# Performance work log

Measured on AMD Instinct MI355X. Metric: run time of the kernel, lower is better.

Reference implementation:

```python
import jax, jax.numpy as jnp
import numpy as np

B, S, IN_DIM = 2048, 65, 256
H, L = 8, 256


def setup_inputs() -> dict:
    key = jax.random.key(0)
    ks = jax.random.split(key, 8)
    return {
        "x": jax.random.normal(ks[0], (B, S, IN_DIM), dtype=jnp.float32),
        "Wq": jax.random.normal(ks[1], (H, IN_DIM, L), dtype=jnp.float32),
        "Wk": jax.random.normal(ks[2], (H, IN_DIM, L), dtype=jnp.float32),
        "Wv": jax.random.normal(ks[3], (H, IN_DIM, L), dtype=jnp.float32),
        "W": jax.random.normal(ks[4], (H, L, 1), dtype=jnp.float32),
        "O": jax.random.normal(ks[5], (H * L, IN_DIM), dtype=jnp.float32),
        "P": jax.random.normal(ks[6], (S - 1, IN_DIM), dtype=jnp.float32),
        "bias": jax.random.normal(ks[7], (H,), dtype=jnp.float32),
    }


def reference(x, Wq, Wk, Wv, W, O, P, bias):
    origin = x[:, 0, :]                       # [B, D]
    walk = x[:, 1:, :]                        # [B, S-1, D]
    origin_seq = origin[:, None, :] + P       # [B, S-1, D]

    # per-head sigmoid projections, vectorized over heads
    k = jax.nn.sigmoid(jnp.einsum('bsd,hdl->bhsl', origin_seq, Wk))
    q = jax.nn.sigmoid(jnp.einsum('bsd,hdl->bhsl', walk, Wq))
    v = jax.nn.sigmoid(jnp.einsum('bsd,hdl->bhsl', walk, Wv))

    edge = jnp.cos(k * q) + bias[None, :, None, None]       # [B,H,S-1,L]
    score = jnp.einsum('bhsl,hl->bhs', edge, W[..., 0])      # [B,H,S-1]
    score = jax.nn.softmax(score, axis=-1)
    res = jnp.einsum('bhs,bhsl->bhl', score, v)              # [B,H,L]
    res = res.reshape(res.shape[0], H * L)                   # concat heads
    out = jax.nn.sigmoid(res @ O)                            # [B, D]
    return jnp.concatenate([out, origin], axis=-1)           # [B, 2D]
```

## Files before the change

kernel.cpp:

```cpp
#include <hip/hip_runtime.h>
#include <math.h>

#define NB   2048
#define NSEQ 65
#define ND   256
#define NH   8
#define NL   256
#define NS   64
#define APAD 264

typedef _Float16 f16;
typedef _Float16 f16x4 __attribute__((ext_vector_type(4)));
typedef _Float16 f16x8 __attribute__((ext_vector_type(8)));
typedef float    f32x4 __attribute__((ext_vector_type(4)));

__device__ __forceinline__ float sigmoidf_(float x) {
    return __builtin_amdgcn_rcpf(1.0f + __expf(-x));
}

__global__ __launch_bounds__(256) void wh_kernel(const float* __restrict__ Wq,
                                                 const float* __restrict__ Wv,
                                                 const float* __restrict__ Wk,
                                                 f16* __restrict__ wh) {
    int hm = blockIdx.x >> 4;
    int h  = hm / 3, m = hm % 3;
    int n  = ((blockIdx.x & 15) << 4) + (threadIdx.x >> 4);
    int kc = (threadIdx.x & 15) << 4;
    const float* src = (m == 0 ? Wq : (m == 1 ? Wv : Wk)) + h * (ND * NL);
    f16x8 t0, t1;
    #pragma unroll
    for (int j = 0; j < 8; ++j) t0[j] = (f16)src[(kc + j) * NL + n];
    #pragma unroll
    for (int j = 0; j < 8; ++j) t1[j] = (f16)src[(kc + 8 + j) * NL + n];
    f16* dst = wh + ((size_t)(hm * 256 + n)) * 256 + kc;
    *(f16x8*)dst       = t0;
    *(f16x8*)(dst + 8) = t1;
}

__global__ __launch_bounds__(256) void ot_kernel(const float* __restrict__ O,
                                                 f16* __restrict__ OT) {
    int n = blockIdx.x;
    int t = threadIdx.x;
    f16x8 v;
    #pragma unroll
    for (int j = 0; j < 8; ++j) v[j] = (f16)O[(size_t)(t * 8 + j) * 256 + n];
    *(f16x8*)(OT + (size_t)n * 2048 + t * 8) = v;
}

__global__ __launch_bounds__(256) void pkt_kernel(const float* __restrict__ P,
                                                  const float* __restrict__ Wk,
                                                  float* __restrict__ PKT) {
    int h = blockIdx.x >> 6;
    int s = blockIdx.x & 63;
    int t = threadIdx.x;
    __shared__ float p_s[ND];
    p_s[t] = P[s * ND + t];
    __syncthreads();
    const float* wk = Wk + h * (ND * NL) + t;
    float acc = 0.f;
    #pragma unroll 8
    for (int d = 0; d < ND; ++d) acc = fmaf(p_s[d], wk[d * NL], acc);
    PKT[((size_t)h * NL + t) * NS + s] = acc;
}

__global__ __launch_bounds__(256) void ok_gemm(const float* __restrict__ x,
                                               const f16*   __restrict__ wh,
                                               float* __restrict__ OK) {
    int mblk = blockIdx.x >> 4;
    int nblk = blockIdx.x & 15;
    int b0 = mblk * 64;
    int h  = nblk >> 1;
    int l0 = (nblk & 1) * 128;
    int t = threadIdx.x;
    int w = t >> 6, lane = t & 63, c = lane & 15, g = lane >> 4;

    __shared__ f16 Ao[64 * APAD];
    #pragma unroll
    for (int it = 0; it < 16; ++it) {
        int idx4 = it * 256 + t;
        int s = idx4 >> 6, kq = idx4 & 63;
        float4 v = *(const float4*)(x + (size_t)(b0 + s) * (NSEQ * ND) + kq * 4);
        *(f16x4*)(&Ao[s * APAD + kq * 4]) = (f16x4){(f16)v.x, (f16)v.y, (f16)v.z, (f16)v.w};
    }
    __syncthreads();

    f32x4 acc[4][2];
    #pragma unroll
    for (int mt = 0; mt < 4; ++mt)
        #pragma unroll
        for (int nt = 0; nt < 2; ++nt) acc[mt][nt] = (f32x4){0.f, 0.f, 0.f, 0.f};

    const f16* bb = wh + ((size_t)((h * 3 + 2) * 256 + l0 + w * 32 + c)) * 256;
    #pragma unroll 2
    for (int kk = 0; kk < 8; ++kk) {
        int k0 = kk * 32 + g * 8;
        f16x8 af[4];
        #pragma unroll
        for (int mt = 0; mt < 4; ++mt)
            af[mt] = *(const f16x8*)(&Ao[(mt * 16 + c) * APAD + k0]);
        #pragma unroll
        for (int nt = 0; nt < 2; ++nt) {
            f16x8 bf = *(const f16x8*)(bb + nt * 16 * 256 + k0);
            #pragma unroll
            for (int mt = 0; mt < 4; ++mt)
                acc[mt][nt] = __builtin_amdgcn_mfma_f32_16x16x32_f16(af[mt], bf, acc[mt][nt], 0, 0, 0);
        }
    }
    #pragma unroll
    for (int mt = 0; mt < 4; ++mt)
        #pragma unroll
        for (int nt = 0; nt < 2; ++nt)
            #pragma unroll
            for (int r = 0; r < 4; ++r)
                OK[((size_t)h * NB + b0 + mt * 16 + g * 4 + r) * NL + l0 + w * 32 + nt * 16 + c]
                    = acc[mt][nt][r];
}

__global__ __launch_bounds__(512, 8) void attn_mfma(
        const float* __restrict__ x,
        const f16*   __restrict__ wh,
        const float* __restrict__ W,
        const float* __restrict__ PKT,
        const float* __restrict__ OK,
        f16* __restrict__ res) {
    int b = blockIdx.x;
    int t = threadIdx.x;
    int w    = t >> 6;
    int lane = t & 63;
    int c = lane & 15;
    int g = lane >> 4;

    __shared__ f16 A[NS * 256];

    const float* xb = x + (size_t)b * (NSEQ * ND);

    #pragma unroll
    for (int it = 0; it < 8; ++it) {
        int idx4 = it * 512 + t;
        int s  = idx4 >> 6;
        int kq = idx4 & 63;
        float4 v = *(const float4*)(xb + (1 + s) * ND + kq * 4);
        int kp = (kq * 4) ^ ((s & 7) << 3);
        *(f16x4*)(&A[s * 256 + kp]) = (f16x4){(f16)v.x, (f16)v.y, (f16)v.z, (f16)v.w};
    }
    __syncthreads();

    int swz = (c & 7) << 3;
    int rot = b & 7;
    int h = w;

    float part[4][4];
    #pragma unroll
    for (int mt = 0; mt < 4; ++mt)
        #pragma unroll
        for (int r = 0; r < 4; ++r) part[mt][r] = 0.f;

    for (int ci = 0; ci < 8; ++ci) {
        int ch = (ci + rot) & 7;
        f32x4 acc[4][2];
        #pragma unroll
        for (int mt = 0; mt < 4; ++mt)
            #pragma unroll
            for (int nt = 0; nt < 2; ++nt) acc[mt][nt] = (f32x4){0.f, 0.f, 0.f, 0.f};

        const f16* bq = wh + ((size_t)((h * 3 + 0) * 256 + ch * 32 + c)) * 256;
        #pragma unroll 2
        for (int kk = 0; kk < 8; ++kk) {
            int k0 = kk * 32 + g * 8;
            f16x8 af[4];
            #pragma unroll
            for (int mt = 0; mt < 4; ++mt)
                af[mt] = *(const f16x8*)(&A[(mt * 16 + c) * 256 + (k0 ^ swz)]);
            #pragma unroll
            for (int nt = 0; nt < 2; ++nt) {
                f16x8 bf = *(const f16x8*)(bq + nt * 16 * 256 + k0);
                #pragma unroll
                for (int mt = 0; mt < 4; ++mt)
                    acc[mt][nt] = __builtin_amdgcn_mfma_f32_16x16x32_f16(af[mt], bf, acc[mt][nt], 0, 0, 0);
            }
        }
        #pragma unroll
        for (int nt = 0; nt < 2; ++nt) {
            int l = ch * 32 + nt * 16 + c;
            float wl  = W[h * NL + l];
            float okv = OK[((size_t)h * NB + b) * NL + l];
            const float* pkcol = PKT + ((size_t)h * NL + l) * NS + g * 4;
            #pragma unroll
            for (int mt = 0; mt < 4; ++mt) {
                float4 pk4 = *(const float4*)(pkcol + mt * 16);
                float pks[4] = {pk4.x, pk4.y, pk4.z, pk4.w};
                #pragma unroll
                for (int r = 0; r < 4; ++r) {
                    float qs = sigmoidf_(acc[mt][nt][r]);
                    float ks = sigmoidf_(okv + pks[r]);
                    part[mt][r] = fmaf(__cosf(ks * qs), wl, part[mt][r]);
                }
            }
        }
    }

    #pragma unroll
    for (int mt = 0; mt < 4; ++mt)
        #pragma unroll
        for (int r = 0; r < 4; ++r) {
            float v = part[mt][r];
            v += __shfl_xor(v, 1, 64);
            v += __shfl_xor(v, 2, 64);
            v += __shfl_xor(v, 4, 64);
            v += __shfl_xor(v, 8, 64);
            part[mt][r] = v;
        }
    float m = part[0][0];
    #pragma unroll
    for (int mt = 0; mt < 4; ++mt)
        #pragma unroll
        for (int r = 0; r < 4; ++r) m = fmaxf(m, part[mt][r]);
    m = fmaxf(m, __shfl_xor(m, 16, 64));
    m = fmaxf(m, __shfl_xor(m, 32, 64));
    float ssum = 0.f;
    #pragma unroll
    for (int mt = 0; mt < 4; ++mt)
        #pragma unroll
        for (int r = 0; r < 4; ++r) {
            float e = __expf(part[mt][r] - m);
            part[mt][r] = e;
            ssum += e;
        }
    ssum += __shfl_xor(ssum, 16, 64);
    ssum += __shfl_xor(ssum, 32, 64);
    float rinv = __builtin_amdgcn_rcpf(ssum);
    #pragma unroll
    for (int mt = 0; mt < 4; ++mt)
        #pragma unroll
        for (int r = 0; r < 4; ++r) part[mt][r] *= rinv;

    for (int ci = 0; ci < 8; ++ci) {
        int ch = (ci + rot) & 7;
        f32x4 acc[4][2];
        #pragma unroll
        for (int mt = 0; mt < 4; ++mt)
            #pragma unroll
            for (int nt = 0; nt < 2; ++nt) acc[mt][nt] = (f32x4){0.f, 0.f, 0.f, 0.f};

        const f16* bv = wh + ((size_t)((h * 3 + 1) * 256 + ch * 32 + c)) * 256;
        #pragma unroll 2
        for (int kk = 0; kk < 8; ++kk) {
            int k0 = kk * 32 + g * 8;
            f16x8 af[4];
            #pragma unroll
            for (int mt = 0; mt < 4; ++mt)
                af[mt] = *(const f16x8*)(&A[(mt * 16 + c) * 256 + (k0 ^ swz)]);
            #pragma unroll
            for (int nt = 0; nt < 2; ++nt) {
                f16x8 bf = *(const f16x8*)(bv + nt * 16 * 256 + k0);
                #pragma unroll
                for (int mt = 0; mt < 4; ++mt)
                    acc[mt][nt] = __builtin_amdgcn_mfma_f32_16x16x32_f16(af[mt], bf, acc[mt][nt], 0, 0, 0);
            }
        }
        #pragma unroll
        for (int nt = 0; nt < 2; ++nt) {
            float v = 0.f;
            #pragma unroll
            for (int mt = 0; mt < 4; ++mt)
                #pragma unroll
                for (int r = 0; r < 4; ++r)
                    v = fmaf(part[mt][r], sigmoidf_(acc[mt][nt][r]), v);
            v += __shfl_xor(v, 16, 64);
            v += __shfl_xor(v, 32, 64);
            if (g == 0)
                res[(size_t)b * 2048 + h * NL + ch * 32 + nt * 16 + c] = (f16)v;
        }
    }
}

__global__ __launch_bounds__(256) void out_gemm(
        const float* __restrict__ x,
        const f16*   __restrict__ res,
        const f16*   __restrict__ OT,
        float* __restrict__ out) {
    int mblk = blockIdx.x >> 1;
    int nblk = blockIdx.x & 1;
    int b0 = mblk * 32;
    int t  = threadIdx.x;
    int w    = t >> 6;
    int lane = t & 63;
    int c = lane & 15;
    int g = lane >> 4;

    __shared__ f16 Ao[32 * APAD];

    f32x4 acc[2][2];
    #pragma unroll
    for (int mt = 0; mt < 2; ++mt)
        #pragma unroll
        for (int nt = 0; nt < 2; ++nt) acc[mt][nt] = (f32x4){0.f, 0.f, 0.f, 0.f};

    for (int chunk = 0; chunk < 8; ++chunk) {
        int kbase = chunk * 256;
        __syncthreads();
        #pragma unroll
        for (int it = 0; it < 4; ++it) {
            int id  = it * 256 + t;
            int row = id >> 5;
            int kc  = (id & 31) << 3;
            *(f16x8*)(&Ao[row * APAD + kc]) =
                *(const f16x8*)(res + (size_t)(b0 + row) * 2048 + kbase + kc);
        }
        __syncthreads();
        #pragma unroll
        for (int kk = 0; kk < 8; ++kk) {
            int k0 = kk * 32 + g * 8;
            f16x8 af[2];
            #pragma unroll
            for (int mt = 0; mt < 2; ++mt)
                af[mt] = *(const f16x8*)(&Ao[(mt * 16 + c) * APAD + k0]);
            #pragma unroll
            for (int nt = 0; nt < 2; ++nt) {
                f16x8 bf = *(const f16x8*)(OT + (size_t)(nblk * 128 + w * 32 + nt * 16 + c) * 2048 + kbase + k0);
                #pragma unroll
                for (int mt = 0; mt < 2; ++mt)
                    acc[mt][nt] = __builtin_amdgcn_mfma_f32_16x16x32_f16(af[mt], bf, acc[mt][nt], 0, 0, 0);
            }
        }
    }
    #pragma unroll
    for (int mt = 0; mt < 2; ++mt)
        #pragma unroll
        for (int nt = 0; nt < 2; ++nt)
            #pragma unroll
            for (int r = 0; r < 4; ++r) {
                int row = mt * 16 + g * 4 + r;
                int col = nblk * 128 + w * 32 + nt * 16 + c;
                out[(size_t)(b0 + row) * 512 + col] = sigmoidf_(acc[mt][nt][r]);
            }
    if (nblk == 1) {
        for (int r2 = 0; r2 < 32; ++r2)
            out[(size_t)(b0 + r2) * 512 + 256 + t] = x[(size_t)(b0 + r2) * (NSEQ * ND) + t];
    }
}

extern "C" void kernel_launch(void* const* d_in, const int* in_sizes, int n_in,
                              void* d_out, int out_size, void* d_ws, size_t ws_size,
                              hipStream_t stream) {
    const float* x    = (const float*)d_in[0];
    const float* Wq   = (const float*)d_in[1];
    const float* Wk   = (const float*)d_in[2];
    const float* Wv   = (const float*)d_in[3];
    const float* W    = (const float*)d_in[4];
    const float* O    = (const float*)d_in[5];
    const float* P    = (const float*)d_in[6];
    float* out = (float*)d_out;

    char* wsb = (char*)d_ws;
    f16*   wh  = (f16*)wsb;
    f16*   OT  = (f16*)(wsb + 3145728);
    float* PKT = (float*)(wsb + 4194304);
    float* OK  = (float*)(wsb + 4718592);
    f16*   res = (f16*)(wsb + 21495808);

    wh_kernel<<<384, 256, 0, stream>>>(Wq, Wv, Wk, wh);
    ot_kernel<<<256, 256, 0, stream>>>(O, OT);
    pkt_kernel<<<NH * NS, 256, 0, stream>>>(P, Wk, PKT);
    ok_gemm<<<512, 256, 0, stream>>>(x, wh, OK);
    attn_mfma<<<NB, 512, 0, stream>>>(x, wh, W, PKT, OK, res);
    out_gemm<<<128, 256, 0, stream>>>(x, res, OT, out);
}
```

Measured before the change: 980.4 us.

## Fold log2e into weights, split attention M-tiles, pad LDS rows

```diff
diff --git a/kernel.cpp b/kernel.cpp
--- a/kernel.cpp
+++ b/kernel.cpp
@@ -8,6 +8,8 @@
 #define NL   256
 #define NS   64
 #define APAD 264
+#define AROW 288
+#define LOG2E 1.44269504088896f
 
 typedef _Float16 f16;
 typedef _Float16 f16x4 __attribute__((ext_vector_type(4)));
@@ -16,6 +18,11 @@
 
 __device__ __forceinline__ float sigmoidf_(float x) {
     return __builtin_amdgcn_rcpf(1.0f + __expf(-x));
+}
+__device__ __forceinline__ float sigmoid2_(float x) {
+    float e;
+    asm("v_exp_f32 %0, -%1" : "=v"(e) : "v"(x));
+    return __builtin_amdgcn_rcpf(1.0f + e);
 }
 
 __global__ __launch_bounds__(256) void wh_kernel(const float* __restrict__ Wq,
@@ -29,9 +36,9 @@
     const float* src = (m == 0 ? Wq : (m == 1 ? Wv : Wk)) + h * (ND * NL);
     f16x8 t0, t1;
     #pragma unroll
-    for (int j = 0; j < 8; ++j) t0[j] = (f16)src[(kc + j) * NL + n];
-    #pragma unroll
-    for (int j = 0; j < 8; ++j) t1[j] = (f16)src[(kc + 8 + j) * NL + n];
+    for (int j = 0; j < 8; ++j) t0[j] = (f16)(src[(kc + j) * NL + n] * LOG2E);
+    #pragma unroll
+    for (int j = 0; j < 8; ++j) t1[j] = (f16)(src[(kc + 8 + j) * NL + n] * LOG2E);
     f16* dst = wh + ((size_t)(hm * 256 + n)) * 256 + kc;
     *(f16x8*)dst       = t0;
     *(f16x8*)(dst + 8) = t1;
@@ -43,7 +50,7 @@
     int t = threadIdx.x;
     f16x8 v;
     #pragma unroll
-    for (int j = 0; j < 8; ++j) v[j] = (f16)O[(size_t)(t * 8 + j) * 256 + n];
+    for (int j = 0; j < 8; ++j) v[j] = (f16)(O[(size_t)(t * 8 + j) * 256 + n] * LOG2E);
     *(f16x8*)(OT + (size_t)n * 2048 + t * 8) = v;
 }
 
@@ -60,7 +67,7 @@
     float acc = 0.f;
     #pragma unroll 8
     for (int d = 0; d < ND; ++d) acc = fmaf(p_s[d], wk[d * NL], acc);
-    PKT[((size_t)h * NL + t) * NS + s] = acc;
+    PKT[((size_t)h * NL + t) * NS + s] = acc * LOG2E;
 }
 
 __global__ __launch_bounds__(256) void ok_gemm(const float* __restrict__ x,
@@ -116,7 +123,7 @@
                     = acc[mt][nt][r];
 }
 
-__global__ __launch_bounds__(512, 8) void attn_mfma(
+__global__ __launch_bounds__(512, 6) void attn_mfma(
         const float* __restrict__ x,
         const f16*   __restrict__ wh,
         const float* __restrict__ W,
@@ -130,7 +137,7 @@
     int c = lane & 15;
     int g = lane >> 4;
 
-    __shared__ f16 A[NS * 256];
+    __shared__ f16 A[NS * AROW];
 
     const float* xb = x + (size_t)b * (NSEQ * ND);
 
@@ -141,7 +148,7 @@
         int kq = idx4 & 63;
         float4 v = *(const float4*)(xb + (1 + s) * ND + kq * 4);
         int kp = (kq * 4) ^ ((s & 7) << 3);
-        *(f16x4*)(&A[s * 256 + kp]) = (f16x4){(f16)v.x, (f16)v.y, (f16)v.z, (f16)v.w};
+        *(f16x4*)(&A[s * AROW + kp]) = (f16x4){(f16)v.x, (f16)v.y, (f16)v.z, (f16)v.w};
     }
     __syncthreads();
 
@@ -155,45 +162,54 @@
         #pragma unroll
         for (int r = 0; r < 4; ++r) part[mt][r] = 0.f;
 
+    #pragma unroll 1
     for (int ci = 0; ci < 8; ++ci) {
         int ch = (ci + rot) & 7;
-        f32x4 acc[4][2];
-        #pragma unroll
-        for (int mt = 0; mt < 4; ++mt)
-            #pragma unroll
-            for (int nt = 0; nt < 2; ++nt) acc[mt][nt] = (f32x4){0.f, 0.f, 0.f, 0.f};
-
         const f16* bq = wh + ((size_t)((h * 3 + 0) * 256 + ch * 32 + c)) * 256;
-        #pragma unroll 2
-        for (int kk = 0; kk < 8; ++kk) {
-            int k0 = kk * 32 + g * 8;
-            f16x8 af[4];
-            #pragma unroll
-            for (int mt = 0; mt < 4; ++mt)
-                af[mt] = *(const f16x8*)(&A[(mt * 16 + c) * 256 + (k0 ^ swz)]);
+        float wl0 = W[h * NL + ch * 32 + c];
+        float wl1 = W[h * NL + ch * 32 + 16 + c];
+        float ok0 = OK[((size_t)h * NB + b) * NL + ch * 32 + c];
+        float ok1 = OK[((size_t)h * NB + b) * NL + ch * 32 + 16 + c];
+
+        #pragma unroll 1
+        for (int mh = 0; mh < 2; ++mh) {
+            f32x4 acc[2][2];
+            #pragma unroll
+            for (int m2 = 0; m2 < 2; ++m2)
+                #pragma unroll
+                for (int nt = 0; nt < 2; ++nt) acc[m2][nt] = (f32x4){0.f, 0.f, 0.f, 0.f};
+
+            #pragma unroll 2
+            for (int kk = 0; kk < 8; ++kk) {
+                int k0 = kk * 32 + g * 8;
+                f16x8 af[2];
+                #pragma unroll
+                for (int m2 = 0; m2 < 2; ++m2)
+                    af[m2] = *(const f16x8*)(&A[(mh * 32 + m2 * 16 + c) * AROW + (k0 ^ swz)]);
+                #pragma unroll
+                for (int nt = 0; nt < 2; ++nt) {
+                    f16x8 bf = *(const f16x8*)(bq + nt * 16 * 256 + k0);
+                    #pragma unroll
+                    for (int m2 = 0; m2 < 2; ++m2)
+                        acc[m2][nt] = __builtin_amdgcn_mfma_f32_16x16x32_f16(af[m2], bf, acc[m2][nt], 0, 0, 0);
+                }
+            }
             #pragma unroll
             for (int nt = 0; nt < 2; ++nt) {
-                f16x8 bf = *(const f16x8*)(bq + nt * 16 * 256 + k0);
-                #pragma unroll
-                for (int mt = 0; mt < 4; ++mt)
-                    acc[mt][nt] = __builtin_amdgcn_mfma_f32_16x16x32_f16(af[mt], bf, acc[mt][nt], 0, 0, 0);
-            }
-        }
-        #pragma unroll
-        for (int nt = 0; nt < 2; ++nt) {
-            int l = ch * 32 + nt * 16 + c;
-            float wl  = W[h * NL + l];
-            float okv = OK[((size_t)h * NB + b) * NL + l];
-            const float* pkcol = PKT + ((size_t)h * NL + l) * NS + g * 4;
-            #pragma unroll
-            for (int mt = 0; mt < 4; ++mt) {
-                float4 pk4 = *(const float4*)(pkcol + mt * 16);
-                float pks[4] = {pk4.x, pk4.y, pk4.z, pk4.w};
-                #pragma unroll
-                for (int r = 0; r < 4; ++r) {
-                    float qs = sigmoidf_(acc[mt][nt][r]);
-                    float ks = sigmoidf_(okv + pks[r]);
-                    part[mt][r] = fmaf(__cosf(ks * qs), wl, part[mt][r]);
+                int l = ch * 32 + nt * 16 + c;
+                float wl  = nt ? wl1 : wl0;
+                float okv = nt ? ok1 : ok0;
+                const float* pkcol = PKT + ((size_t)h * NL + l) * NS + mh * 32 + g * 4;
+                #pragma unroll
+                for (int m2 = 0; m2 < 2; ++m2) {
+                    float4 pk4 = *(const float4*)(pkcol + m2 * 16);
+                    float pks[4] = {pk4.x, pk4.y, pk4.z, pk4.w};
+                    #pragma unroll
+                    for (int r = 0; r < 4; ++r) {
+                        float qs = sigmoid2_(acc[m2][nt][r]);
+                        float ks = sigmoid2_(okv + pks[r]);
+                        part[mh * 2 + m2][r] = fmaf(__cosf(ks * qs), wl, part[mh * 2 + m2][r]);
+                    }
                 }
             }
         }
@@ -234,38 +250,46 @@
         #pragma unroll
         for (int r = 0; r < 4; ++r) part[mt][r] *= rinv;
 
+    #pragma unroll 1
     for (int ci = 0; ci < 8; ++ci) {
         int ch = (ci + rot) & 7;
-        f32x4 acc[4][2];
-        #pragma unroll
-        for (int mt = 0; mt < 4; ++mt)
-            #pragma unroll
-            for (int nt = 0; nt < 2; ++nt) acc[mt][nt] = (f32x4){0.f, 0.f, 0.f, 0.f};
-
         const f16* bv = wh + ((size_t)((h * 3 + 1) * 256 + ch * 32 + c)) * 256;
-        #pragma unroll 2
-        for (int kk = 0; kk < 8; ++kk) {
-            int k0 = kk * 32 + g * 8;
-            f16x8 af[4];
-            #pragma unroll
-            for (int mt = 0; mt < 4; ++mt)
-                af[mt] = *(const f16x8*)(&A[(mt * 16 + c) * 256 + (k0 ^ swz)]);
-            #pragma unroll
-            for (int nt = 0; nt < 2; ++nt) {
-                f16x8 bf = *(const f16x8*)(bv + nt * 16 * 256 + k0);
-                #pragma unroll
-                for (int mt = 0; mt < 4; ++mt)
-                    acc[mt][nt] = __builtin_amdgcn_mfma_f32_16x16x32_f16(af[mt], bf, acc[mt][nt], 0, 0, 0);
-            }
+        float vsum[2] = {0.f, 0.f};
+
+        #pragma unroll 1
+        for (int mh = 0; mh < 2; ++mh) {
+            f32x4 acc[2][2];
+            #pragma unroll
+            for (int m2 = 0; m2 < 2; ++m2)
+                #pragma unroll
+                for (int nt = 0; nt < 2; ++nt) acc[m2][nt] = (f32x4){0.f, 0.f, 0.f, 0.f};
+
+            #pragma unroll 2
+            for (int kk = 0; kk < 8; ++kk) {
+                int k0 = kk * 32 + g * 8;
+                f16x8 af[2];
+                #pragma unroll
+                for (int m2 = 0; m2 < 2; ++m2)
+                    af[m2] = *(const f16x8*)(&A[(mh * 32 + m2 * 16 + c) * AROW + (k0 ^ swz)]);
+                #pragma unroll
+                for (int nt = 0; nt < 2; ++nt) {
+                    f16x8 bf = *(const f16x8*)(bv + nt * 16 * 256 + k0);
+                    #pragma unroll
+                    for (int m2 = 0; m2 < 2; ++m2)
+                        acc[m2][nt] = __builtin_amdgcn_mfma_f32_16x16x32_f16(af[m2], bf, acc[m2][nt], 0, 0, 0);
+                }
+            }
+            #pragma unroll
+            for (int nt = 0; nt < 2; ++nt)
+                #pragma unroll
+                for (int m2 = 0; m2 < 2; ++m2)
+                    #pragma unroll
+                    for (int r = 0; r < 4; ++r)
+                        vsum[nt] = fmaf(part[mh * 2 + m2][r], sigmoid2_(acc[m2][nt][r]), vsum[nt]);
         }
         #pragma unroll
         for (int nt = 0; nt < 2; ++nt) {
-            float v = 0.f;
-            #pragma unroll
-            for (int mt = 0; mt < 4; ++mt)
-                #pragma unroll
-                for (int r = 0; r < 4; ++r)
-                    v = fmaf(part[mt][r], sigmoidf_(acc[mt][nt][r]), v);
+            float v = vsum[nt];
             v += __shfl_xor(v, 16, 64);
             v += __shfl_xor(v, 32, 64);
             if (g == 0)
@@ -332,7 +356,7 @@
             for (int r = 0; r < 4; ++r) {
                 int row = mt * 16 + g * 4 + r;
                 int col = nblk * 128 + w * 32 + nt * 16 + c;
-                out[(size_t)(b0 + row) * 512 + col] = sigmoidf_(acc[mt][nt][r]);
+                out[(size_t)(b0 + row) * 512 + col] = sigmoid2_(acc[mt][nt][r]);
             }
     if (nblk == 1) {
         for (int r2 = 0; r2 < 32; ++r2)
```

After: 1.427 ms. 45.6% more time.
